# Optimization experiments

Hardware: AMD Instinct MI355X
Metric: run time of the kernel (lower is better)

Reference implementation:

```python
import jax, jax.numpy as jnp
import numpy as np
from jax import lax

EPS = 1e-5

def _conv(x, w, pad):
    return lax.conv_general_dilated(
        x, w, window_strides=(1, 1), padding=[(pad, pad), (pad, pad)],
        dimension_numbers=('NCHW', 'OIHW', 'NCHW'))

def _bn(x, p):
    # p: [4, C] rows = gamma, beta, running_mean, running_var (inference BN)
    g, b, m, v = p[0], p[1], p[2], p[3]
    scale = g / jnp.sqrt(v + EPS)
    return x * scale[None, :, None, None] + (b - m * scale)[None, :, None, None]

def _cbr(x, w, p, relu=True):
    y = _bn(_conv(x, w, pad=1), p)
    return jax.nn.relu(y) if relu else y

def _make_bn(key, c):
    k1, k2, k3 = jax.random.split(key, 3)
    gamma = jnp.ones((c,), jnp.float32) + 0.05 * jax.random.normal(k1, (c,))
    beta = 0.1 * jax.random.normal(k2, (c,))
    mean = 0.1 * jax.random.normal(k3, (c,))
    var = jax.random.uniform(k1, (c,), minval=0.5, maxval=1.5)
    return jnp.stack([gamma, beta, mean, var]).astype(jnp.float32)

def setup_inputs() -> dict:
    key = jax.random.key(0)
    ks = jax.random.split(key, 12)
    C, M = 256, 64  # channels, bottleneck width (hard-coded 64 in source)
    B, H, W = 8, 128, 128
    s = lambda fan: 1.0 / np.sqrt(fan)
    return {
        'x': jax.random.normal(ks[0], (B, C, H, W), jnp.float32),
        'w_res': jax.random.normal(ks[1], (C, C, 1, 1), jnp.float32) * s(C),
        'bn_res': _make_bn(ks[2], C),
        'w_vpre': jax.random.normal(ks[3], (M, C, 3, 3), jnp.float32) * s(C * 9),
        'bn_vpre': _make_bn(ks[4], M),
        'w_hpre': jax.random.normal(ks[5], (M, C, 3, 3), jnp.float32) * s(C * 9),
        'bn_hpre': _make_bn(ks[6], M),
        'w_add': jax.random.normal(ks[7], (C, M, 3, 3), jnp.float32) * s(M * 9),
        'bn_add': _make_bn(ks[8], C),
        'w_post': jax.random.normal(ks[9], (C, C, 3, 3), jnp.float32) * s(C * 9),
        'bn_post': _make_bn(ks[10], C),
    }

def reference(x, w_res, bn_res, w_vpre, bn_vpre, w_hpre, bn_hpre,
              w_add, bn_add, w_post, bn_post):
    # residual branch: 1x1 conv + BN (no relu)
    res = _bn(_conv(x, w_res, pad=0), bn_res)
    # vertical branch: conv-bn-relu then TopPool (reverse cumulative max over H)
    p1 = _cbr(x, w_vpre, bn_vpre)
    pool1 = lax.cummax(p1, axis=2, reverse=True)
    # horizontal branch: conv-bn-relu then LeftPool (reverse cumulative max over W)
    p2 = _cbr(x, w_hpre, bn_hpre)
    pool2 = lax.cummax(p2, axis=3, reverse=True)
    # merge: conv-bn (no relu), residual add, relu, post conv-bn-relu
    merged = _cbr(pool1 + pool2, w_add, bn_add, relu=False)
    out = jax.nn.relu(res + merged)
    return _cbr(out, w_post, bn_post)
```

## Files before the change

### kernel.cpp

```cpp
#include <hip/hip_runtime.h>
#include <hip/hip_bf16.h>


using bf16x8  = __attribute__((ext_vector_type(8))) __bf16;
using floatx4 = __attribute__((ext_vector_type(4))) float;

typedef __attribute__((address_space(1))) const uint32_t gas_u32;
typedef __attribute__((address_space(3))) uint32_t las_u32;

__device__ __forceinline__ float bf2f(__hip_bfloat16 h) { return __bfloat162float(h); }
__device__ __forceinline__ __hip_bfloat16 f2bf(float f) { return __float2bfloat16(f); }


__global__ __launch_bounds__(256) void k_cast_x(const float* __restrict__ x,
                                                __hip_bfloat16* __restrict__ xb) {
    __shared__ float t[64][65];
    const int n  = blockIdx.z;
    const int h  = blockIdx.y;
    const int c0 = (blockIdx.x >> 1) * 64;
    const int w0 = (blockIdx.x & 1) * 64;
    const int tid = threadIdx.x;
#pragma unroll
    for (int it = 0; it < 16; ++it) {
        int idx = it * 256 + tid;
        int c = idx >> 6, w = idx & 63;
        t[c][w] = x[(((size_t)n * 256 + c0 + c) * 128 + h) * 128 + w0 + w];
    }
    __syncthreads();
#pragma unroll
    for (int it = 0; it < 16; ++it) {
        int idx = it * 256 + tid;
        int w = idx >> 6, c = idx & 63;
        xb[(((size_t)n * 128 + h) * 128 + w0 + w) * 256 + c0 + c] = f2bf(t[c][w]);
    }
}

__global__ void k_prep_bn(const float* __restrict__ p, float* __restrict__ sc,
                          float* __restrict__ bi, int C) {
    int i = blockIdx.x * 64 + threadIdx.x;
    if (i >= C) return;
    float g = p[i], b = p[C + i], m = p[2 * C + i], v = p[3 * C + i];
    float s = g / sqrtf(v + 1e-5f);
    sc[i] = s;
    bi[i] = b - m * s;
}

__global__ void k_reorder_w3(const float* __restrict__ src, __hip_bfloat16* __restrict__ dst,
                             const float* __restrict__ scale, int Cin, int CoutTot,
                             int co_off, int total) {
    int i = blockIdx.x * 256 + threadIdx.x;
    if (i >= total) return;
    int ci  = i % Cin;
    int tap = (i / Cin) % 9;
    int co  = i / (Cin * 9);
    dst[((((size_t)tap * (Cin >> 5) + (ci >> 5)) * CoutTot) + co_off + co) * 32 + (ci & 31)] =
        f2bf(src[((size_t)co * Cin + ci) * 9 + tap] * scale[co]);
}

__global__ void k_reorder_w1(const float* __restrict__ src, __hip_bfloat16* __restrict__ dst,
                             const float* __restrict__ scale, int Cin, int total) {
    int i = blockIdx.x * 256 + threadIdx.x;
    if (i >= total) return;
    dst[i] = f2bf(src[i] * scale[i / Cin]);
}


__global__ __launch_bounds__(256) void k_pool1(__hip_bfloat16* __restrict__ b) {
    const int idx = blockIdx.x * 256 + threadIdx.x;
    const int c = idx & 63;
    const int w = (idx >> 6) & 127;
    const int n = idx >> 13;
    const size_t stride = 128 * 64;
    const size_t base = ((size_t)n * 128 * 128 + w) * 64 + c;
    float m = 0.0f;
    for (int hb = 31; hb >= 0; --hb) {
        size_t a0 = base + (size_t)(4 * hb) * stride;
        float v0 = bf2f(b[a0]);
        float v1 = bf2f(b[a0 + stride]);
        float v2 = bf2f(b[a0 + 2 * stride]);
        float v3 = bf2f(b[a0 + 3 * stride]);
        float m3 = fmaxf(m, v3);
        float m2 = fmaxf(m3, v2);
        float m1 = fmaxf(m2, v1);
        float m0 = fmaxf(m1, v0);
        b[a0 + 3 * stride] = f2bf(m3);
        b[a0 + 2 * stride] = f2bf(m2);
        b[a0 + stride]     = f2bf(m1);
        b[a0]              = f2bf(m0);
        m = m0;
    }
}

__global__ __launch_bounds__(256) void k_pool2(__hip_bfloat16* __restrict__ b,
                                               const __hip_bfloat16* __restrict__ pl) {
    const int idx = blockIdx.x * 256 + threadIdx.x;
    const int c = idx & 63;
    const int h = (idx >> 6) & 127;
    const int n = idx >> 13;
    const size_t base = (((size_t)n * 128 + h) * 128) * 64 + c;
    float m = 0.0f;
    for (int wb = 31; wb >= 0; --wb) {
        size_t a0 = base + (size_t)(4 * wb) * 64;
        float v0 = bf2f(b[a0]);
        float v1 = bf2f(b[a0 + 64]);
        float v2 = bf2f(b[a0 + 128]);
        float v3 = bf2f(b[a0 + 192]);
        float u0 = bf2f(pl[a0]);
        float u1 = bf2f(pl[a0 + 64]);
        float u2 = bf2f(pl[a0 + 128]);
        float u3 = bf2f(pl[a0 + 192]);
        float m3 = fmaxf(m, v3);
        float m2 = fmaxf(m3, v2);
        float m1 = fmaxf(m2, v1);
        float m0 = fmaxf(m1, v0);
        b[a0 + 192] = f2bf(m3 + u3);
        b[a0 + 128] = f2bf(m2 + u2);
        b[a0 + 64]  = f2bf(m1 + u1);
        b[a0]       = f2bf(m0 + u0);
        m = m0;
    }
}

__global__ __launch_bounds__(256) void conv1x1(const __hip_bfloat16* __restrict__ xin,
                                               const __hip_bfloat16* __restrict__ wgt,
                                               const float* __restrict__ bias,
                                               __hip_bfloat16* __restrict__ out) {
    __shared__ __align__(16) __hip_bfloat16 Xs[128 * 64];
    __shared__ __align__(16) __hip_bfloat16 Ws[128 * 64];
    const int tid  = threadIdx.x;
    const int lane = tid & 63;
    const int wid  = tid >> 6;
    const int wm = wid >> 1, wn = wid & 1;
    const int p0 = blockIdx.x * 128;
    const int c0 = blockIdx.y * 128;
    const int q = lane >> 4, r16 = lane & 15;

    floatx4 acc[4][4] = {};

    for (int k0 = 0; k0 < 256; k0 += 64) {
#pragma unroll
        for (int it = 0; it < 4; ++it) {
            const int pp = it * 32 + (tid >> 3);
            const int g  = tid & 7;
            uint4 val = *(const uint4*)(xin + ((size_t)(p0 + pp) * 256 + k0 + g * 8));
            *(uint4*)(&Xs[pp * 64 + (((g + pp) & 7) * 8)]) = val;
        }
#pragma unroll
        for (int it = 0; it < 4; ++it) {
            const int rr = it * 32 + (tid >> 3);
            const int g  = tid & 7;
            uint4 val = *(const uint4*)(wgt + ((size_t)(c0 + rr) * 256 + k0 + g * 8));
            *(uint4*)(&Ws[rr * 64 + (((g + rr) & 7) * 8)]) = val;
        }
        __syncthreads();
#pragma unroll
        for (int ks = 0; ks < 2; ++ks) {
            bf16x8 afr[4], bfr[4];
#pragma unroll
            for (int i = 0; i < 4; ++i) {
                const int pp = wm * 64 + i * 16 + r16;
                const int g  = ks * 4 + q;
                afr[i] = *(const bf16x8*)(&Xs[pp * 64 + (((g + pp) & 7) * 8)]);
            }
#pragma unroll
            for (int j = 0; j < 4; ++j) {
                const int rr = wn * 64 + j * 16 + r16;
                const int g  = ks * 4 + q;
                bfr[j] = *(const bf16x8*)(&Ws[rr * 64 + (((g + rr) & 7) * 8)]);
            }
#pragma unroll
            for (int i = 0; i < 4; ++i)
#pragma unroll
                for (int j = 0; j < 4; ++j)
                    acc[i][j] = __builtin_amdgcn_mfma_f32_16x16x32_bf16(afr[i], bfr[j], acc[i][j], 0, 0, 0);
        }
        __syncthreads();
    }
#pragma unroll
    for (int j = 0; j < 4; ++j) {
        const int co = c0 + wn * 64 + j * 16 + r16;
        const float bi = bias[co];
#pragma unroll
        for (int i = 0; i < 4; ++i) {
            const int pb = p0 + wm * 64 + i * 16 + q * 4;
#pragma unroll
            for (int r = 0; r < 4; ++r)
                out[(size_t)(pb + r) * 256 + co] = f2bf(acc[i][j][r] + bi);
        }
    }
}

template <int CIN, int COUT, int MODE>
__global__ __launch_bounds__(512, 2) void conv3x3(const __hip_bfloat16* __restrict__ xin,
                                                  const __hip_bfloat16* __restrict__ wgt,
                                                  const float* __restrict__ bias,
                                                  void* __restrict__ out,
                                                  const __hip_bfloat16* __restrict__ resbuf,
                                                  __hip_bfloat16* __restrict__ out2) {
    constexpr int NCH = CIN / 32;
    __shared__ __align__(16) __hip_bfloat16 Xs[6 * 130 * 32];
    __shared__ __align__(16) __hip_bfloat16 Ws[9 * 128 * 32];
    const int tid  = threadIdx.x;
    const int lane = tid & 63;
    const int wid  = tid >> 6;
    const int wm   = wid >> 1;
    const int wn   = wid & 1;
    const int bx   = blockIdx.x;
    const int n     = bx >> 5;
    const int hbase = (bx & 31) * 4;
    const int co_off = blockIdx.y * 128;
    const int q = lane >> 4, r16 = lane & 15;

    const int le = lane >> 2, lp = lane & 3;
    const int xe = wid * 16 + 1 + le;
    const int xg = (lp - ((xe >> 1) & 3)) & 3;
    const int xlaneoff = (xe - 1) * CIN + xg * 8;
    const int wrow = wid * 16 + le;
    const int wg2 = (lp - ((wrow >> 1) & 3)) & 3;
    const int wlaneoff = wrow * 32 + wg2 * 8;

    floatx4 acc[4][2][4] = {};

    auto stage = [&](int c) {
        const int ci0 = c * 32;
#pragma unroll
        for (int r = 0; r < 6; ++r) {
            const int hh = hbase - 1 + r;
            if (0 <= hh && hh < 128) {
                const __hip_bfloat16* src =
                    xin + ((size_t)(n * 128 + hh) * 128) * CIN + ci0 + xlaneoff;
                __builtin_amdgcn_global_load_lds((gas_u32*)src,
                    (las_u32*)&Xs[((size_t)r * 130 + wid * 16 + 1) * 32], 16, 0, 0);
            } else {
                *(uint4*)(&Xs[((size_t)r * 130 + xe) * 32 + lp * 8]) =
                    make_uint4(0u, 0u, 0u, 0u);
            }
        }
#pragma unroll
        for (int tap = 0; tap < 9; ++tap) {
            const __hip_bfloat16* src =
                wgt + ((size_t)(tap * NCH + c) * COUT + co_off) * 32 + wlaneoff;
            __builtin_amdgcn_global_load_lds((gas_u32*)src,
                (las_u32*)&Ws[((size_t)tap * 128 + wid * 16) * 32], 16, 0, 0);
        }
    };

    if (tid < 48) {
        int r = tid >> 3, side = (tid >> 2) & 1, p = tid & 3;
        *(uint4*)(&Xs[((size_t)r * 130 + (side ? 129 : 0)) * 32 + p * 8]) =
            make_uint4(0u, 0u, 0u, 0u);
    }
    const int off = (bx >> 3) % NCH;
    stage(off);
    __syncthreads();

    for (int c = 0; c < NCH; ++c) {
#pragma unroll
        for (int dwg = 0; dwg < 3; ++dwg) {
            const int dw = dwg - 1;
            bf16x8 bfr[3][4];
#pragma unroll
            for (int tr = 0; tr < 3; ++tr)
#pragma unroll
                for (int j = 0; j < 4; ++j) {
                    const int row = wn * 64 + j * 16 + r16;
                    const int pg  = (q + ((row >> 1) & 3)) & 3;
                    bfr[tr][j] = *(const bf16x8*)(
                        &Ws[((size_t)(tr * 3 + dwg) * 128 + row) * 32 + pg * 8]);
                }
#pragma unroll
            for (int i = 0; i < 2; ++i) {
                const int e  = wm * 32 + i * 16 + r16 + dw + 1;
                const int pg = (q + ((e >> 1) & 3)) & 3;
                bf16x8 afr[6];
#pragma unroll
                for (int rr = 0; rr < 6; ++rr)
                    afr[rr] = *(const bf16x8*)(
                        &Xs[((size_t)rr * 130 + e) * 32 + pg * 8]);
#pragma unroll
                for (int tr = 0; tr < 3; ++tr)
#pragma unroll
                    for (int row = 0; row < 4; ++row)
#pragma unroll
                        for (int j = 0; j < 4; ++j) {
                            if (MODE == 3)
                                acc[row][i][j] = __builtin_amdgcn_mfma_f32_16x16x32_bf16(
                                    bfr[tr][j], afr[row + tr], acc[row][i][j], 0, 0, 0);
                            else
                                acc[row][i][j] = __builtin_amdgcn_mfma_f32_16x16x32_bf16(
                                    afr[row + tr], bfr[tr][j], acc[row][i][j], 0, 0, 0);
                        }
            }
        }
        __syncthreads();
        if (c + 1 < NCH) {
            stage((c + 1 + off) % NCH);
            __syncthreads();
        }
    }

    if (MODE == 1) {
#pragma unroll
        for (int row = 0; row < 4; ++row) {
            const int h = hbase + row;
#pragma unroll
            for (int j = 0; j < 4; ++j) {
                const int co = wn * 64 + j * 16 + r16;
                const float bi = bias[co];
                __hip_bfloat16* ob = (co < 64) ? (__hip_bfloat16*)out : out2;
                const int ch = co & 63;
#pragma unroll
                for (int i = 0; i < 2; ++i) {
#pragma unroll
                    for (int r = 0; r < 4; ++r) {
                        const int w = wm * 32 + i * 16 + q * 4 + r;
                        const size_t p = (size_t)(n * 128 + h) * 128 + w;
                        ob[p * 64 + ch] = f2bf(fmaxf(acc[row][i][j][r] + bi, 0.0f));
                    }
                }
            }
        }
    } else if (MODE == 2) {
        __hip_bfloat16* o = (__hip_bfloat16*)out;
#pragma unroll
        for (int row = 0; row < 4; ++row) {
            const int h = hbase + row;
#pragma unroll
            for (int j = 0; j < 4; ++j) {
                const int co = co_off + wn * 64 + j * 16 + r16;
                const float bi = bias[co];
#pragma unroll
                for (int i = 0; i < 2; ++i) {
#pragma unroll
                    for (int r = 0; r < 4; ++r) {
                        const int w = wm * 32 + i * 16 + q * 4 + r;
                        const size_t p = (size_t)(n * 128 + h) * 128 + w;
                        float v = acc[row][i][j][r] + bi + bf2f(resbuf[p * 256 + co]);
                        o[p * 256 + co] = f2bf(fmaxf(v, 0.0f));
                    }
                }
            }
        }
    } else {
        float* o = (float*)out;
#pragma unroll
        for (int row = 0; row < 4; ++row) {
            const int h = hbase + row;
#pragma unroll
            for (int j = 0; j < 4; ++j) {
#pragma unroll
                for (int r = 0; r < 4; ++r) {
                    const int co = co_off + wn * 64 + j * 16 + q * 4 + r;
                    const float bi = bias[co];
#pragma unroll
                    for (int i = 0; i < 2; ++i) {
                        const int w = wm * 32 + i * 16 + r16;
                        float v = fmaxf(acc[row][i][j][r] + bi, 0.0f);
                        o[(((size_t)(n * 256 + co)) * 128 + h) * 128 + w] = v;
                    }
                }
            }
        }
    }
}


extern "C" void kernel_launch(void* const* d_in, const int* in_sizes, int n_in,
                              void* d_out, int out_size, void* d_ws, size_t ws_size,
                              hipStream_t stream) {
    const float* x       = (const float*)d_in[0];
    const float* w_res   = (const float*)d_in[1];
    const float* bn_res  = (const float*)d_in[2];
    const float* w_vpre  = (const float*)d_in[3];
    const float* bn_vpre = (const float*)d_in[4];
    const float* w_hpre  = (const float*)d_in[5];
    const float* bn_hpre = (const float*)d_in[6];
    const float* w_add   = (const float*)d_in[7];
    const float* bn_add  = (const float*)d_in[8];
    const float* w_post  = (const float*)d_in[9];
    const float* bn_post = (const float*)d_in[10];

    const size_t SZ_XB = (size_t)8 * 128 * 128 * 256 * 2;
    const size_t SZ_P  = (size_t)8 * 128 * 128 * 64 * 2;

    char* w = (char*)d_ws;
    __hip_bfloat16* xb   = (__hip_bfloat16*)(w);
    __hip_bfloat16* resb = (__hip_bfloat16*)(w + SZ_XB);
    __hip_bfloat16* p1   = (__hip_bfloat16*)(w + 2 * SZ_XB);
    __hip_bfloat16* p2   = (__hip_bfloat16*)(w + 2 * SZ_XB + SZ_P);
    char* wp = w + 2 * SZ_XB + 2 * SZ_P;
    __hip_bfloat16* wres  = (__hip_bfloat16*)wp; wp += (size_t)65536 * 2;
    __hip_bfloat16* wpre  = (__hip_bfloat16*)wp; wp += (size_t)9 * 128 * 256 * 2;
    __hip_bfloat16* wadd  = (__hip_bfloat16*)wp; wp += (size_t)9 * 256 * 64 * 2;
    __hip_bfloat16* wpost = (__hip_bfloat16*)wp; wp += (size_t)9 * 256 * 256 * 2;
    float* sc_res  = (float*)wp; wp += 256 * 4;
    float* bi_res  = (float*)wp; wp += 256 * 4;
    float* sc_pre  = (float*)wp; wp += 128 * 4;
    float* bi_pre  = (float*)wp; wp += 128 * 4;
    float* sc_add  = (float*)wp; wp += 256 * 4;
    float* bi_add  = (float*)wp; wp += 256 * 4;
    float* sc_post = (float*)wp; wp += 256 * 4;
    float* bi_post = (float*)wp; wp += 256 * 4;

    k_prep_bn<<<4, 64, 0, stream>>>(bn_res, sc_res, bi_res, 256);
    k_prep_bn<<<1, 64, 0, stream>>>(bn_vpre, sc_pre, bi_pre, 64);
    k_prep_bn<<<1, 64, 0, stream>>>(bn_hpre, sc_pre + 64, bi_pre + 64, 64);
    k_prep_bn<<<4, 64, 0, stream>>>(bn_add, sc_add, bi_add, 256);
    k_prep_bn<<<4, 64, 0, stream>>>(bn_post, sc_post, bi_post, 256);

    k_reorder_w1<<<256, 256, 0, stream>>>(w_res, wres, sc_res, 256, 65536);
    k_reorder_w3<<<576, 256, 0, stream>>>(w_vpre, wpre, sc_pre, 256, 128, 0, 147456);
    k_reorder_w3<<<576, 256, 0, stream>>>(w_hpre, wpre, sc_pre + 64, 256, 128, 64, 147456);
    k_reorder_w3<<<576, 256, 0, stream>>>(w_add, wadd, sc_add, 64, 256, 0, 147456);
    k_reorder_w3<<<2304, 256, 0, stream>>>(w_post, wpost, sc_post, 256, 256, 0, 589824);

    k_cast_x<<<dim3(8, 128, 8), 256, 0, stream>>>(x, xb);

    conv1x1<<<dim3(1024, 2), 256, 0, stream>>>(xb, wres, bi_res, resb);
    conv3x3<256, 128, 1><<<dim3(256, 1), 512, 0, stream>>>(xb, wpre, bi_pre, p1, nullptr, p2);
    k_pool1<<<256, 256, 0, stream>>>(p1);
    k_pool2<<<256, 256, 0, stream>>>(p2, p1);
    conv3x3<64, 256, 2><<<dim3(256, 2), 512, 0, stream>>>(p2, wadd, bi_add, xb, resb, nullptr);
    conv3x3<256, 256, 3><<<dim3(256, 2), 512, 0, stream>>>(xb, wpost, bi_post, d_out, nullptr, nullptr);
}
```

Baseline: 374.2 us.

## Shrink conv3x3 tiles to 2 rows, 256 threads, stage weights per tap column

The 3x3 convolution kernel moves from 512-thread blocks covering 4 output rows to 256-thread blocks covering 2 rows, each wave now handling 64 columns. Shared memory is cut by staging only 4 input rows and only the 3 taps for the current horizontal offset, instead of all 9 taps at once. The aim is lower LDS use and more blocks per CU for better occupancy and SM coverage. The cost is an extra pair of barriers per tap group with no double buffering, plus more input-row redundancy (4 rows loaded for 2 outputs).

```diff
diff --git a/kernel.cpp b/kernel.cpp
--- a/kernel.cpp
+++ b/kernel.cpp
@@ -191,117 +191,126 @@
 }
 
 template <int CIN, int COUT, int MODE>
-__global__ __launch_bounds__(512, 2) void conv3x3(const __hip_bfloat16* __restrict__ xin,
+__global__ __launch_bounds__(256, 2) void conv3x3(const __hip_bfloat16* __restrict__ xin,
                                                   const __hip_bfloat16* __restrict__ wgt,
                                                   const float* __restrict__ bias,
                                                   void* __restrict__ out,
                                                   const __hip_bfloat16* __restrict__ resbuf,
                                                   __hip_bfloat16* __restrict__ out2) {
     constexpr int NCH = CIN / 32;
-    __shared__ __align__(16) __hip_bfloat16 Xs[6 * 130 * 32];
-    __shared__ __align__(16) __hip_bfloat16 Ws[9 * 128 * 32];
+    __shared__ __align__(16) __hip_bfloat16 Xs[4 * 130 * 32];
+    __shared__ __align__(16) __hip_bfloat16 Ws[3 * 128 * 32];
     const int tid  = threadIdx.x;
     const int lane = tid & 63;
     const int wid  = tid >> 6;
     const int wm   = wid >> 1;
     const int wn   = wid & 1;
     const int bx   = blockIdx.x;
-    const int n     = bx >> 5;
-    const int hbase = (bx & 31) * 4;
+    const int n     = bx >> 6;
+    const int hbase = (bx & 63) * 2;
     const int co_off = blockIdx.y * 128;
     const int q = lane >> 4, r16 = lane & 15;
 
-    const int le = lane >> 2, lp = lane & 3;
-    const int xe = wid * 16 + 1 + le;
-    const int xg = (lp - ((xe >> 1) & 3)) & 3;
-    const int xlaneoff = (xe - 1) * CIN + xg * 8;
-    const int wrow = wid * 16 + le;
-    const int wg2 = (lp - ((wrow >> 1) & 3)) & 3;
-    const int wlaneoff = wrow * 32 + wg2 * 8;
-
-    floatx4 acc[4][2][4] = {};
-
-    auto stage = [&](int c) {
+    const int le = lane >> 2;
+    const int gq = lane & 3;
+
+    floatx4 acc[2][4][4] = {};
+
+    auto stageX = [&](int c) {
         const int ci0 = c * 32;
 #pragma unroll
-        for (int r = 0; r < 6; ++r) {
-            const int hh = hbase - 1 + r;
+        for (int it = 0; it < 8; ++it) {
+            const int cid = it * 4 + wid;
+            const int row = cid >> 3;
+            const int m   = cid & 7;
+            const int e0  = m * 16 + 1;
+            const int hh  = hbase - 1 + row;
+            const int e   = e0 + le;
+            const int g   = (gq - ((e >> 1) & 3)) & 3;
             if (0 <= hh && hh < 128) {
                 const __hip_bfloat16* src =
-                    xin + ((size_t)(n * 128 + hh) * 128) * CIN + ci0 + xlaneoff;
+                    xin + ((size_t)(n * 128 + hh) * 128 + (e - 1)) * CIN + ci0 + g * 8;
                 __builtin_amdgcn_global_load_lds((gas_u32*)src,
-                    (las_u32*)&Xs[((size_t)r * 130 + wid * 16 + 1) * 32], 16, 0, 0);
+                    (las_u32*)&Xs[((size_t)row * 130 + e0) * 32], 16, 0, 0);
             } else {
-                *(uint4*)(&Xs[((size_t)r * 130 + xe) * 32 + lp * 8]) =
+                *(uint4*)(&Xs[((size_t)row * 130 + e) * 32 + gq * 8]) =
                     make_uint4(0u, 0u, 0u, 0u);
             }
         }
-#pragma unroll
-        for (int tap = 0; tap < 9; ++tap) {
+    };
+    auto stageW = [&](int c, int dwg) {
+#pragma unroll
+        for (int it = 0; it < 6; ++it) {
+            const int cid  = it * 4 + wid;
+            const int tr   = cid >> 3;
+            const int m    = cid & 7;
+            const int row0 = m * 16;
+            const int wrow = row0 + le;
+            const int g    = (gq - ((wrow >> 1) & 3)) & 3;
+            const int tap  = tr * 3 + dwg;
             const __hip_bfloat16* src =
-                wgt + ((size_t)(tap * NCH + c) * COUT + co_off) * 32 + wlaneoff;
+                wgt + ((size_t)(tap * NCH + c) * COUT + co_off + wrow) * 32 + g * 8;
             __builtin_amdgcn_global_load_lds((gas_u32*)src,
-                (las_u32*)&Ws[((size_t)tap * 128 + wid * 16) * 32], 16, 0, 0);
+                (las_u32*)&Ws[((size_t)tr * 128 + row0) * 32], 16, 0, 0);
         }
     };
-
-    if (tid < 48) {
-        int r = tid >> 3, side = (tid >> 2) & 1, p = tid & 3;
-        *(uint4*)(&Xs[((size_t)r * 130 + (side ? 129 : 0)) * 32 + p * 8]) =
+    auto tapsg = [&](int dwg) {
+        const int dw = dwg - 1;
+        bf16x8 bfr[3][4];
+#pragma unroll
+        for (int tr = 0; tr < 3; ++tr)
+#pragma unroll
+            for (int j = 0; j < 4; ++j) {
+                const int row = wn * 64 + j * 16 + r16;
+                const int pg  = (q + ((row >> 1) & 3)) & 3;
+                bfr[tr][j] = *(const bf16x8*)(&Ws[((size_t)tr * 128 + row) * 32 + pg * 8]);
+            }
+#pragma unroll
+        for (int i = 0; i < 4; ++i) {
+            const int e  = wm * 64 + i * 16 + r16 + dw + 1;
+            const int pg = (q + ((e >> 1) & 3)) & 3;
+            bf16x8 afr[4];
+#pragma unroll
+            for (int rr = 0; rr < 4; ++rr)
+                afr[rr] = *(const bf16x8*)(&Xs[((size_t)rr * 130 + e) * 32 + pg * 8]);
+#pragma unroll
+            for (int tr = 0; tr < 3; ++tr)
+#pragma unroll
+                for (int row = 0; row < 2; ++row)
+#pragma unroll
+                    for (int j = 0; j < 4; ++j) {
+                        if (MODE == 3)
+                            acc[row][i][j] = __builtin_amdgcn_mfma_f32_16x16x32_bf16(
+                                bfr[tr][j], afr[row + tr], acc[row][i][j], 0, 0, 0);
+                        else
+                            acc[row][i][j] = __builtin_amdgcn_mfma_f32_16x16x32_bf16(
+                                afr[row + tr], bfr[tr][j], acc[row][i][j], 0, 0, 0);
+                    }
+        }
+    };
+
+    if (tid < 32) {
+        int row = tid >> 3, side = (tid >> 2) & 1, p = tid & 3;
+        *(uint4*)(&Xs[((size_t)row * 130 + (side ? 129 : 0)) * 32 + p * 8]) =
             make_uint4(0u, 0u, 0u, 0u);
     }
     const int off = (bx >> 3) % NCH;
-    stage(off);
-    __syncthreads();
 
     for (int c = 0; c < NCH; ++c) {
+        const int cc = (c + off) % NCH;
 #pragma unroll
         for (int dwg = 0; dwg < 3; ++dwg) {
-            const int dw = dwg - 1;
-            bf16x8 bfr[3][4];
-#pragma unroll
-            for (int tr = 0; tr < 3; ++tr)
-#pragma unroll
-                for (int j = 0; j < 4; ++j) {
-                    const int row = wn * 64 + j * 16 + r16;
-                    const int pg  = (q + ((row >> 1) & 3)) & 3;
-                    bfr[tr][j] = *(const bf16x8*)(
-                        &Ws[((size_t)(tr * 3 + dwg) * 128 + row) * 32 + pg * 8]);
-                }
-#pragma unroll
-            for (int i = 0; i < 2; ++i) {
-                const int e  = wm * 32 + i * 16 + r16 + dw + 1;
-                const int pg = (q + ((e >> 1) & 3)) & 3;
-                bf16x8 afr[6];
-#pragma unroll
-                for (int rr = 0; rr < 6; ++rr)
-                    afr[rr] = *(const bf16x8*)(
-                        &Xs[((size_t)rr * 130 + e) * 32 + pg * 8]);
-#pragma unroll
-                for (int tr = 0; tr < 3; ++tr)
-#pragma unroll
-                    for (int row = 0; row < 4; ++row)
-#pragma unroll
-                        for (int j = 0; j < 4; ++j) {
-                            if (MODE == 3)
-                                acc[row][i][j] = __builtin_amdgcn_mfma_f32_16x16x32_bf16(
-                                    bfr[tr][j], afr[row + tr], acc[row][i][j], 0, 0, 0);
-                            else
-                                acc[row][i][j] = __builtin_amdgcn_mfma_f32_16x16x32_bf16(
-                                    afr[row + tr], bfr[tr][j], acc[row][i][j], 0, 0, 0);
-                        }
-            }
-        }
-        __syncthreads();
-        if (c + 1 < NCH) {
-            stage((c + 1 + off) % NCH);
+            if (dwg == 0) stageX(cc);
+            stageW(cc, dwg);
             __syncthreads();
+            tapsg(dwg);
+            __syncthreads();
         }
     }
 
     if (MODE == 1) {
 #pragma unroll
-        for (int row = 0; row < 4; ++row) {
+        for (int row = 0; row < 2; ++row) {
             const int h = hbase + row;
 #pragma unroll
             for (int j = 0; j < 4; ++j) {
@@ -310,10 +319,10 @@
                 __hip_bfloat16* ob = (co < 64) ? (__hip_bfloat16*)out : out2;
                 const int ch = co & 63;
 #pragma unroll
-                for (int i = 0; i < 2; ++i) {
+                for (int i = 0; i < 4; ++i) {
 #pragma unroll
                     for (int r = 0; r < 4; ++r) {
-                        const int w = wm * 32 + i * 16 + q * 4 + r;
+                        const int w = wm * 64 + i * 16 + q * 4 + r;
                         const size_t p = (size_t)(n * 128 + h) * 128 + w;
                         ob[p * 64 + ch] = f2bf(fmaxf(acc[row][i][j][r] + bi, 0.0f));
                     }
@@ -323,17 +332,17 @@
     } else if (MODE == 2) {
         __hip_bfloat16* o = (__hip_bfloat16*)out;
 #pragma unroll
-        for (int row = 0; row < 4; ++row) {
+        for (int row = 0; row < 2; ++row) {
             const int h = hbase + row;
 #pragma unroll
             for (int j = 0; j < 4; ++j) {
                 const int co = co_off + wn * 64 + j * 16 + r16;
                 const float bi = bias[co];
 #pragma unroll
-                for (int i = 0; i < 2; ++i) {
+                for (int i = 0; i < 4; ++i) {
 #pragma unroll
                     for (int r = 0; r < 4; ++r) {
-                        const int w = wm * 32 + i * 16 + q * 4 + r;
+                        const int w = wm * 64 + i * 16 + q * 4 + r;
                         const size_t p = (size_t)(n * 128 + h) * 128 + w;
                         float v = acc[row][i][j][r] + bi + bf2f(resbuf[p * 256 + co]);
                         o[p * 256 + co] = f2bf(fmaxf(v, 0.0f));
@@ -344,7 +353,7 @@
     } else {
         float* o = (float*)out;
 #pragma unroll
-        for (int row = 0; row < 4; ++row) {
+        for (int row = 0; row < 2; ++row) {
             const int h = hbase + row;
 #pragma unroll
             for (int j = 0; j < 4; ++j) {
@@ -353,8 +362,8 @@
                     const int co = co_off + wn * 64 + j * 16 + q * 4 + r;
                     const float bi = bias[co];
 #pragma unroll
-                    for (int i = 0; i < 2; ++i) {
-                        const int w = wm * 32 + i * 16 + r16;
+                    for (int i = 0; i < 4; ++i) {
+                        const int w = wm * 64 + i * 16 + r16;
                         float v = fmaxf(acc[row][i][j][r] + bi, 0.0f);
                         o[(((size_t)(n * 256 + co)) * 128 + h) * 128 + w] = v;
                     }
@@ -417,9 +426,9 @@
     k_cast_x<<<dim3(8, 128, 8), 256, 0, stream>>>(x, xb);
 
     conv1x1<<<dim3(1024, 2), 256, 0, stream>>>(xb, wres, bi_res, resb);
-    conv3x3<256, 128, 1><<<dim3(256, 1), 512, 0, stream>>>(xb, wpre, bi_pre, p1, nullptr, p2);
+    conv3x3<256, 128, 1><<<dim3(512, 1), 256, 0, stream>>>(xb, wpre, bi_pre, p1, nullptr, p2);
     k_pool1<<<256, 256, 0, stream>>>(p1);
     k_pool2<<<256, 256, 0, stream>>>(p2, p1);
-    conv3x3<64, 256, 2><<<dim3(256, 2), 512, 0, stream>>>(p2, wadd, bi_add, xb, resb, nullptr);
-    conv3x3<256, 256, 3><<<dim3(256, 2), 512, 0, stream>>>(xb, wpost, bi_post, d_out, nullptr, nullptr);
-}
+    conv3x3<64, 256, 2><<<dim3(512, 2), 256, 0, stream>>>(p2, wadd, bi_add, xb, resb, nullptr);
+    conv3x3<256, 256, 3><<<dim3(512, 2), 256, 0, stream>>>(xb, wpost, bi_post, d_out, nullptr, nullptr);
+}
```

Result: slower. 381.9 us (+2.0%).
